# Performance work log

Measured on AMD Instinct MI355X. Metric: run time of the kernel, lower is better.

The kernel has to match this reference:

```python
import jax, jax.numpy as jnp
import numpy as np

B, C, H, W = 8, 256, 64, 64
S = H * W  # dim_spatial = 4096
DQK = 256
DV = 256


def setup_inputs() -> dict:
    key = jax.random.key(0)
    k1, k2, k3, k4, k5 = jax.random.split(key, 5)
    queries = jax.random.normal(k1, (B, DQK, H, W), dtype=jnp.float32)
    keys = jax.random.normal(k2, (B, DQK, H, W), dtype=jnp.float32)
    values = jax.random.normal(k3, (B, DV, H, W), dtype=jnp.float32)
    q_pos = jax.random.normal(k4, (1, S, DQK), dtype=jnp.float32) * 0.05  # 'random_normal' init
    k_pos = jax.random.normal(k5, (1, S, DQK), dtype=jnp.float32) * 0.05
    return {"queries": queries, "keys": keys, "values": values, "q_pos": q_pos, "k_pos": k_pos}


def reference(queries, keys, values, q_pos, k_pos):
    scale = DQK ** (-0.5)
    # NCHW -> (B, S, C)
    q = jnp.transpose(queries, (0, 2, 3, 1)).reshape(-1, S, DQK) + q_pos
    k = jnp.transpose(keys, (0, 2, 3, 1)).reshape(-1, S, DQK) + k_pos
    v = jnp.transpose(values, (0, 2, 3, 1)).reshape(-1, S, DV)
    dots = jnp.einsum('bqd,bkd->bqk', q, k) * scale  # (B, S, S)
    attn = jax.nn.softmax(dots, axis=-1)
    out = jnp.einsum('bqk,bkd->bqd', attn, v)  # (B, S, DV)
    out = jnp.transpose(out, (0, 2, 1)).reshape(values.shape)  # (B, DV, H, W)
    return out
```

## Files before the change

### kernel.cpp

```cpp
#include <hip/hip_runtime.h>
#include <hip/hip_bf16.h>

#define B_N   8
#define S_N   4096
#define D_N   256
#define QBLK  128
#define KVBLK 32
#define NCH   (S_N / KVBLK)
#define IMGSZ 16384
#define SCALE_Q (0.0625f * 1.4426950408889634f)

typedef __attribute__((ext_vector_type(8)))  short bf16x8;
typedef __attribute__((ext_vector_type(16))) float f32x16;

__device__ __forceinline__ void async16(const char* g, char* l) {
  __builtin_amdgcn_global_load_lds(
      (const __attribute__((address_space(1))) void*)g,
      (__attribute__((address_space(3))) void*)l, 16, 0, 0);
}

__device__ __forceinline__ unsigned cvt_pk_bf16(float lo, float hi) {
  unsigned r;
  asm("v_cvt_pk_bf16_f32 %0, %1, %2" : "=v"(r) : "v"(lo), "v"(hi));
  return r;
}
__device__ __forceinline__ void swap32(unsigned& a, unsigned& b) {
  asm("v_permlane32_swap_b32 %0, %1" : "+v"(a), "+v"(b));
}
__device__ __forceinline__ float xhalf_max(float x) {
  float a = x, b = x;
  asm("" : "+v"(b));
  asm("v_permlane32_swap_b32 %0, %1" : "+v"(a), "+v"(b));
  return fmaxf(a, b);
}
__device__ __forceinline__ float xhalf_add(float x) {
  float a = x, b = x;
  asm("" : "+v"(b));
  asm("v_permlane32_swap_b32 %0, %1" : "+v"(a), "+v"(b));
  return a + b;
}
__device__ __forceinline__ float exp2_fast(float x) {
  float r;
  asm("v_exp_f32 %0, %1" : "=v"(r) : "v"(x));
  return r;
}

__global__ void prep_qk(const float* __restrict__ src, const float* __restrict__ pos,
                        __hip_bfloat16* __restrict__ dst, float mul) {
  __shared__ float tile[64][65];
  const int b  = blockIdx.z;
  const int s0 = blockIdx.x * 64;
  const int c0 = blockIdx.y * 64;
  const int t  = threadIdx.x;
  const int x  = t & 63;
  const int y4 = t >> 6;
  const float* sp = src + ((size_t)b * D_N + c0) * S_N + s0;
#pragma unroll
  for (int i = 0; i < 16; ++i) {
    int c = y4 + i * 4;
    tile[c][x] = sp[(size_t)c * S_N + x];
  }
  __syncthreads();
  __hip_bfloat16* dp = dst + ((size_t)b * S_N + s0) * D_N + c0;
  const float* pp = pos + (size_t)s0 * D_N + c0;
#pragma unroll
  for (int i = 0; i < 16; ++i) {
    int s = y4 + i * 4;
    float v = (tile[x][s] + pp[(size_t)s * D_N + x]) * mul;
    dp[(size_t)s * D_N + x] = __float2bfloat16(v);
  }
}

__global__ void prep_kimg(const float* __restrict__ src, const float* __restrict__ pos,
                          char* __restrict__ img) {
  __shared__ float tile[64][65];
  const int b  = blockIdx.z;
  const int s0 = blockIdx.x * 64;
  const int c0 = blockIdx.y * 64;
  const int t  = threadIdx.x;
  const int x  = t & 63;
  const int y4 = t >> 6;
  const float* sp = src + ((size_t)b * D_N + c0) * S_N + s0;
#pragma unroll
  for (int i = 0; i < 16; ++i) {
    int c = y4 + i * 4;
    tile[c][x] = sp[(size_t)c * S_N + x];
  }
  __syncthreads();
  const float* pp = pos + (size_t)s0 * D_N + c0;
#pragma unroll
  for (int i = 0; i < 16; ++i) {
    int srow = y4 + i * 4;
    int d    = c0 + x;
    float v  = tile[x][srow] + pp[(size_t)srow * D_N + x];
    int s    = s0 + srow;
    int ch   = s >> 5;
    char* dst = img + ((size_t)(b * NCH + ch)) * IMGSZ
                + (d >> 4) * 1024 + (s & 31) * 32 + (d & 15) * 2;
    *reinterpret_cast<__hip_bfloat16*>(dst) = __float2bfloat16(v);
  }
}

struct alignas(16) bf8s { __hip_bfloat16 v[8]; };
__global__ void prep_vimg(const float* __restrict__ src, char* __restrict__ img) {
  const int ch = blockIdx.x;
  const int b  = blockIdx.y;
  const int t  = threadIdx.x;
  char* ib = img + ((size_t)(b * NCH + ch)) * IMGSZ;
#pragma unroll
  for (int i = 0; i < 4; ++i) {
    int idx = i * 256 + t;
    int kf  = idx >> 9;
    int d   = (idx >> 1) & 255;
    int hf  = idx & 1;
    const float* vs = src + ((size_t)b * D_N + d) * S_N + ch * KVBLK + kf * 16 + hf * 8;
    float4 a = *reinterpret_cast<const float4*>(vs);
    float4 c = *reinterpret_cast<const float4*>(vs + 4);
    bf8s w;
    w.v[0] = __float2bfloat16(a.x); w.v[1] = __float2bfloat16(a.y);
    w.v[2] = __float2bfloat16(a.z); w.v[3] = __float2bfloat16(a.w);
    w.v[4] = __float2bfloat16(c.x); w.v[5] = __float2bfloat16(c.y);
    w.v[6] = __float2bfloat16(c.z); w.v[7] = __float2bfloat16(c.w);
    *reinterpret_cast<bf8s*>(ib + kf * 8192 + d * 32 + hf * 16) = w;
  }
}

#define LDS_BYTES 65536

__global__ __launch_bounds__(256, 2) void attn_kernel(
    const __hip_bfloat16* __restrict__ Qb, const char* __restrict__ Kt,
    const char* __restrict__ Vt, float* __restrict__ P0,
    float2* __restrict__ mlbuf, float* __restrict__ out) {
  __shared__ __align__(16) char lds[LDS_BYTES];

  const int tid  = threadIdx.x;
  const int wave = tid >> 6;
  const int lane = tid & 63;
  const int l31  = lane & 31;
  const int h    = lane >> 5;
  const int lofs = l31 * 32 + h * 16;

  const int lin = blockIdx.x;
  const int b   = lin & 7;
  const int kvh = (lin >> 3) & 1;
  const int qt  = lin >> 4;
  const int q0  = qt * QBLK + wave * 32;
  const int t0  = kvh * (NCH / 2);

  bf16x8 qf[16];
  {
    const __hip_bfloat16* qp = Qb + ((size_t)b * S_N + q0 + l31) * D_N + h * 8;
#pragma unroll
    for (int kc = 0; kc < 16; ++kc)
      qf[kc] = *reinterpret_cast<const bf16x8*>(qp + kc * 16);
  }

  f32x16 o[8];
#pragma unroll
  for (int df = 0; df < 8; ++df)
#pragma unroll
    for (int r = 0; r < 16; ++r) o[df][r] = 0.f;
  float m_ = -1e30f, l_ = 0.f;

  const char* kimgB = Kt + (size_t)b * NCH * IMGSZ;
  const char* vimgB = Vt + (size_t)b * NCH * IMGSZ;

  auto COMPUTE = [&](const char* Kbase, const char* Vbase) {
    f32x16 se;
#pragma unroll
    for (int r = 0; r < 16; ++r) se[r] = 0.f;
    {
      const char* kr = Kbase + lofs;
#pragma unroll
      for (int kc = 0; kc < 16; ++kc) {
        bf16x8 kf8 = *reinterpret_cast<const bf16x8*>(kr + kc * 1024);
        se = __builtin_amdgcn_mfma_f32_32x32x16_bf16(kf8, qf[kc], se, 0, 0, 0);
      }
    }

    float t8[8];
#pragma unroll
    for (int i = 0; i < 8; ++i) t8[i] = fmaxf(se[i], se[i + 8]);
    float pm = fmaxf(fmaxf(fmaxf(t8[0], t8[1]), fmaxf(t8[2], t8[3])),
                     fmaxf(fmaxf(t8[4], t8[5]), fmaxf(t8[6], t8[7])));
    float pmax = xhalf_max(pm);

    if (!__all(pmax <= m_ + 11.54f)) {
      float mn = fmaxf(m_, pmax);
      float al = exp2_fast(m_ - mn);
      m_ = mn;
      l_ *= al;
#pragma unroll
      for (int df = 0; df < 8; ++df)
#pragma unroll
        for (int r = 0; r < 16; ++r) o[df][r] *= al;
    }
#pragma unroll
    for (int r = 0; r < 16; ++r) se[r] = exp2_fast(se[r] - m_);
    float s8[8];
#pragma unroll
    for (int i = 0; i < 8; ++i) s8[i] = se[i] + se[i + 8];
    float rs = ((s8[0] + s8[1]) + (s8[2] + s8[3])) + ((s8[4] + s8[5]) + (s8[6] + s8[7]));
    l_ += xhalf_add(rs);

    union U8 { unsigned u[4]; bf16x8 v; };
    U8 pb[2];
    {
      unsigned u0 = cvt_pk_bf16(se[0],  se[1]);
      unsigned v0 = cvt_pk_bf16(se[4],  se[5]);
      swap32(u0, v0);
      unsigned u1 = cvt_pk_bf16(se[2],  se[3]);
      unsigned v1 = cvt_pk_bf16(se[6],  se[7]);
      swap32(u1, v1);
      pb[0].u[0] = u0; pb[0].u[1] = u1; pb[0].u[2] = v0; pb[0].u[3] = v1;
      unsigned u2 = cvt_pk_bf16(se[8],  se[9]);
      unsigned v2 = cvt_pk_bf16(se[12], se[13]);
      swap32(u2, v2);
      unsigned u3 = cvt_pk_bf16(se[10], se[11]);
      unsigned v3 = cvt_pk_bf16(se[14], se[15]);
      swap32(u3, v3);
      pb[1].u[0] = u2; pb[1].u[1] = u3; pb[1].u[2] = v2; pb[1].u[3] = v3;
    }

    {
      const char* vr = Vbase + lofs;
#pragma unroll
      for (int df = 0; df < 8; ++df) {
        bf16x8 vf0 = *reinterpret_cast<const bf16x8*>(vr + df * 1024);
        bf16x8 vf1 = *reinterpret_cast<const bf16x8*>(vr + 8192 + df * 1024);
        o[df] = __builtin_amdgcn_mfma_f32_32x32x16_bf16(vf0, pb[0].v, o[df], 0, 0, 0);
        o[df] = __builtin_amdgcn_mfma_f32_32x32x16_bf16(vf1, pb[1].v, o[df], 0, 0, 0);
      }
    }
  };

  for (int t = 0; t < NCH / 4; ++t) {
    __syncthreads();
    {
      const int ch = t0 + 2 * t + (wave & 1);
      const char* s = (wave < 2 ? kimgB : vimgB) + (size_t)ch * IMGSZ;
      char* dstb = lds + (wave < 2 ? 0 : 32768) + (wave & 1) * 16384;
#pragma unroll
      for (int c = 0; c < 16; ++c)
        async16(s + c * 1024 + lane * 16, dstb + c * 1024);
    }
    __syncthreads();

    COMPUTE(lds,         lds + 32768);
    COMPUTE(lds + 16384, lds + 49152);
  }

  if (h == 0)
    mlbuf[(size_t)(kvh * B_N + b) * S_N + q0 + l31] = make_float2(m_, l_);
  float* pdst = (kvh ? out : P0) + (size_t)b * D_N * S_N + q0 + l31;
#pragma unroll
  for (int df = 0; df < 8; ++df)
#pragma unroll
    for (int r = 0; r < 16; ++r) {
      int d = df * 32 + (r & 3) + 8 * (r >> 2) + 4 * h;
      pdst[(size_t)d * S_N] = o[df][r];
    }
}

__global__ void merge_w(const float2* __restrict__ mlbuf, float2* __restrict__ wbuf) {
  int i = blockIdx.x * 256 + threadIdx.x;
  float2 a = mlbuf[i];
  float2 c = mlbuf[(size_t)B_N * S_N + i];
  float ms = fmaxf(a.x, c.x);
  float c0 = exp2f(a.x - ms), c1 = exp2f(c.x - ms);
  float inv = 1.0f / (c0 * a.y + c1 * c.y);
  wbuf[i] = make_float2(c0 * inv, c1 * inv);
}

__global__ void merge_o(const float* __restrict__ P0, const float2* __restrict__ wbuf,
                        float* __restrict__ out) {
  int i = blockIdx.x * 256 + threadIdx.x;
  float4 p0 = reinterpret_cast<const float4*>(P0)[i];
  float4 p1 = reinterpret_cast<float4*>(out)[i];
  int b  = i >> 18;
  int s4 = i & (S_N / 4 - 1);
  const float2* wb = wbuf + (size_t)b * S_N + s4 * 4;
  float2 w0 = wb[0], w1 = wb[1], w2 = wb[2], w3 = wb[3];
  float4 r;
  r.x = w0.x * p0.x + w0.y * p1.x;
  r.y = w1.x * p0.y + w1.y * p1.y;
  r.z = w2.x * p0.z + w2.y * p1.z;
  r.w = w3.x * p0.w + w3.y * p1.w;
  reinterpret_cast<float4*>(out)[i] = r;
}

extern "C" void kernel_launch(void* const* d_in, const int* in_sizes, int n_in,
                              void* d_out, int out_size, void* d_ws, size_t ws_size,
                              hipStream_t stream) {
  const float* queries = (const float*)d_in[0];
  const float* keys    = (const float*)d_in[1];
  const float* values  = (const float*)d_in[2];
  const float* q_pos   = (const float*)d_in[3];
  const float* k_pos   = (const float*)d_in[4];
  float* out = (float*)d_out;

  const size_t per = (size_t)B_N * S_N * D_N;
  __hip_bfloat16* Qb = (__hip_bfloat16*)d_ws;
  char*   Kt    = (char*)d_ws + per * 2;
  char*   Vt    = Kt + per * 2;
  float*  P0    = (float*)(Vt + per * 2);
  float2* mlbuf = (float2*)((char*)P0 + per * 4);
  float2* wbuf  = mlbuf + (size_t)2 * B_N * S_N;

  prep_qk  <<<dim3(S_N / 64, D_N / 64, B_N), 256, 0, stream>>>(queries, q_pos, Qb, SCALE_Q);
  prep_kimg<<<dim3(S_N / 64, D_N / 64, B_N), 256, 0, stream>>>(keys,    k_pos, Kt);
  prep_vimg<<<dim3(NCH, B_N), 256, 0, stream>>>(values, Vt);
  attn_kernel<<<dim3((S_N / QBLK) * B_N * 2), 256, 0, stream>>>(Qb, Kt, Vt, P0, mlbuf, out);
  merge_w<<<dim3(B_N * S_N / 256), 256, 0, stream>>>(mlbuf, wbuf);
  merge_o<<<dim3((unsigned)(per / 4 / 256)), 256, 0, stream>>>(P0, wbuf, out);
}
```

Measured before the change: 193.5 us.

## Store first KV-half partial output as bf16, add setprio and nontemporal stores

The partial output of the first KV half is now stored as bf16 instead of fp32, which halves that intermediate buffer's write and read traffic in attn_kernel and merge_o. Epilogue stores use nontemporal hints, and the MFMA loops are wrapped in s_setprio to favour the matrix-issuing waves. The cost is extra rounding error on half of the unnormalised partial sums. The bf16 stores are scattered 2-byte writes, which may coalesce poorly.

```diff
diff --git a/kernel.cpp b/kernel.cpp
--- a/kernel.cpp
+++ b/kernel.cpp
@@ -43,6 +43,11 @@
   float r;
   asm("v_exp_f32 %0, %1" : "=v"(r) : "v"(x));
   return r;
+}
+__device__ __forceinline__ unsigned short bf16_bits(float x) {
+  union { __hip_bfloat16 h; unsigned short u; } cvt;
+  cvt.h = __float2bfloat16(x);
+  return cvt.u;
 }
 
 __global__ void prep_qk(const float* __restrict__ src, const float* __restrict__ pos,
@@ -129,7 +134,7 @@
 
 __global__ __launch_bounds__(256, 2) void attn_kernel(
     const __hip_bfloat16* __restrict__ Qb, const char* __restrict__ Kt,
-    const char* __restrict__ Vt, float* __restrict__ P0,
+    const char* __restrict__ Vt, __hip_bfloat16* __restrict__ P0,
     float2* __restrict__ mlbuf, float* __restrict__ out) {
   __shared__ __align__(16) char lds[LDS_BYTES];
 
@@ -171,11 +176,13 @@
     for (int r = 0; r < 16; ++r) se[r] = 0.f;
     {
       const char* kr = Kbase + lofs;
+      __builtin_amdgcn_s_setprio(1);
 #pragma unroll
       for (int kc = 0; kc < 16; ++kc) {
         bf16x8 kf8 = *reinterpret_cast<const bf16x8*>(kr + kc * 1024);
         se = __builtin_amdgcn_mfma_f32_32x32x16_bf16(kf8, qf[kc], se, 0, 0, 0);
       }
+      __builtin_amdgcn_s_setprio(0);
     }
 
     float t8[8];
@@ -224,6 +231,7 @@
 
     {
       const char* vr = Vbase + lofs;
+      __builtin_amdgcn_s_setprio(1);
 #pragma unroll
       for (int df = 0; df < 8; ++df) {
         bf16x8 vf0 = *reinterpret_cast<const bf16x8*>(vr + df * 1024);
@@ -231,6 +239,7 @@
         o[df] = __builtin_amdgcn_mfma_f32_32x32x16_bf16(vf0, pb[0].v, o[df], 0, 0, 0);
         o[df] = __builtin_amdgcn_mfma_f32_32x32x16_bf16(vf1, pb[1].v, o[df], 0, 0, 0);
       }
+      __builtin_amdgcn_s_setprio(0);
     }
   };
 
@@ -252,14 +261,26 @@
 
   if (h == 0)
     mlbuf[(size_t)(kvh * B_N + b) * S_N + q0 + l31] = make_float2(m_, l_);
-  float* pdst = (kvh ? out : P0) + (size_t)b * D_N * S_N + q0 + l31;
-#pragma unroll
-  for (int df = 0; df < 8; ++df)
-#pragma unroll
-    for (int r = 0; r < 16; ++r) {
-      int d = df * 32 + (r & 3) + 8 * (r >> 2) + 4 * h;
-      pdst[(size_t)d * S_N] = o[df][r];
-    }
+  if (kvh) {
+    float* pdst = out + (size_t)b * D_N * S_N + q0 + l31;
+#pragma unroll
+    for (int df = 0; df < 8; ++df)
+#pragma unroll
+      for (int r = 0; r < 16; ++r) {
+        int d = df * 32 + (r & 3) + 8 * (r >> 2) + 4 * h;
+        __builtin_nontemporal_store(o[df][r], pdst + (size_t)d * S_N);
+      }
+  } else {
+    unsigned short* pdst = reinterpret_cast<unsigned short*>(P0)
+                           + (size_t)b * D_N * S_N + q0 + l31;
+#pragma unroll
+    for (int df = 0; df < 8; ++df)
+#pragma unroll
+      for (int r = 0; r < 16; ++r) {
+        int d = df * 32 + (r & 3) + 8 * (r >> 2) + 4 * h;
+        __builtin_nontemporal_store(bf16_bits(o[df][r]), pdst + (size_t)d * S_N);
+      }
+  }
 }
 
 __global__ void merge_w(const float2* __restrict__ mlbuf, float2* __restrict__ wbuf) {
@@ -272,20 +293,21 @@
   wbuf[i] = make_float2(c0 * inv, c1 * inv);
 }
 
-__global__ void merge_o(const float* __restrict__ P0, const float2* __restrict__ wbuf,
-                        float* __restrict__ out) {
+__global__ void merge_o(const __hip_bfloat16* __restrict__ P0,
+                        const float2* __restrict__ wbuf, float* __restrict__ out) {
   int i = blockIdx.x * 256 + threadIdx.x;
-  float4 p0 = reinterpret_cast<const float4*>(P0)[i];
+  ushort4 p0u = reinterpret_cast<const ushort4*>(P0)[i];
   float4 p1 = reinterpret_cast<float4*>(out)[i];
   int b  = i >> 18;
   int s4 = i & (S_N / 4 - 1);
   const float2* wb = wbuf + (size_t)b * S_N + s4 * 4;
   float2 w0 = wb[0], w1 = wb[1], w2 = wb[2], w3 = wb[3];
+  union { unsigned short u; __hip_bfloat16 h; } cvt;
   float4 r;
-  r.x = w0.x * p0.x + w0.y * p1.x;
-  r.y = w1.x * p0.y + w1.y * p1.y;
-  r.z = w2.x * p0.z + w2.y * p1.z;
-  r.w = w3.x * p0.w + w3.y * p1.w;
+  cvt.u = p0u.x; r.x = w0.x * __bfloat162float(cvt.h) + w0.y * p1.x;
+  cvt.u = p0u.y; r.y = w1.x * __bfloat162float(cvt.h) + w1.y * p1.y;
+  cvt.u = p0u.z; r.z = w2.x * __bfloat162float(cvt.h) + w2.y * p1.z;
+  cvt.u = p0u.w; r.w = w3.x * __bfloat162float(cvt.h) + w3.y * p1.w;
   reinterpret_cast<float4*>(out)[i] = r;
 }
 
@@ -303,8 +325,8 @@
   __hip_bfloat16* Qb = (__hip_bfloat16*)d_ws;
   char*   Kt    = (char*)d_ws + per * 2;
   char*   Vt    = Kt + per * 2;
-  float*  P0    = (float*)(Vt + per * 2);
-  float2* mlbuf = (float2*)((char*)P0 + per * 4);
+  __hip_bfloat16* P0 = (__hip_bfloat16*)(Vt + per * 2);
+  float2* mlbuf = (float2*)((char*)P0 + per * 2);
   float2* wbuf  = mlbuf + (size_t)2 * B_N * S_N;
 
   prep_qk  <<<dim3(S_N / 64, D_N / 64, B_N), 256, 0, stream>>>(queries, q_pos, Qb, SCALE_Q);
```

Measured after the change: 192.5 us. About the same (-0.5%).
